# Kernel tuning notes

Measured on AMD Instinct MI355X. Metric: run time of the kernel, lower is better.

## Reference

```python
import jax, jax.numpy as jnp
import numpy as np

B, N, D_IN, D_OUT, MAX_POS = 256, 256, 768, 300, 256
NEG_INF = -9e15
LEAKY_SLOPE = 0.2


def setup_inputs() -> dict:
    key = jax.random.key(0)
    ks = jax.random.split(key, 6)
    h = jax.random.normal(ks[0], (B, N, D_IN), dtype=jnp.float32)
    adj = (jax.random.uniform(ks[1], (B, N, N)) > 0.9).astype(jnp.float32)
    adj = jnp.maximum(adj, jnp.eye(N, dtype=jnp.float32)[None])
    positions = jax.random.randint(ks[2], (B, N), 0, MAX_POS)
    W = jax.random.normal(ks[3], (D_IN, D_OUT), dtype=jnp.float32) * (1.0 / np.sqrt(D_IN))
    a_src = jax.random.normal(ks[4], (1, D_OUT), dtype=jnp.float32) * 0.05
    a_dst = jax.random.normal(ks[5], (1, D_OUT), dtype=jnp.float32) * 0.05
    pos_table = jax.random.normal(jax.random.fold_in(key, 7), (MAX_POS, D_OUT), dtype=jnp.float32)
    return {"h": h, "adj": adj, "positions": positions, "W": W,
            "a_src": a_src, "a_dst": a_dst, "pos_table": pos_table}


def reference(h, adj, positions, W, a_src, a_dst, pos_table):
    # Wh = W(h) + position embedding          [B, N, D_OUT]
    Wh = jnp.einsum('bni,io->bno', h, W) + pos_table[positions]
    # additive attention scores
    f_src = jnp.einsum('bno,o->bn', Wh, a_src[0])  # [B, N]
    f_dst = jnp.einsum('bno,o->bn', Wh, a_dst[0])  # [B, N]
    e = f_src[:, :, None] + f_dst[:, None, :]      # [B, N, N]
    e = jnp.where(e >= 0, e, LEAKY_SLOPE * e)      # LeakyReLU(0.2)
    # adjacency masking + softmax over last dim
    masked = jnp.where(adj > 0, e, NEG_INF)
    attention = jax.nn.softmax(masked, axis=-1)
    # (eval mode: edge dropout and dropout are identity)
    h_prime = jnp.einsum('bnm,bmo->bno', attention, Wh)
    return h_prime, attention
```

## Files before the change

kernel.cpp:

```cpp
#include <hip/hip_runtime.h>

#define B_    256
#define N_    256
#define DIN   768
#define DOUT  300
#define DOUTP 320
#define NT    20
#define M_    (B_*N_)
#define HP_ELEMS (M_*DOUT)
#define NEG_INF -9.0e15f

typedef _Float16 f16;
typedef __attribute__((ext_vector_type(8))) _Float16 f16x8;
typedef __attribute__((ext_vector_type(4))) _Float16 f16x4;
typedef __attribute__((ext_vector_type(4))) float    f32x4;

__device__ __forceinline__ void async_copy16(void* lds, const void* g) {
    __builtin_amdgcn_global_load_lds(
        (const __attribute__((address_space(1))) void*)g,
        (__attribute__((address_space(3))) void*)lds, 16, 0, 0);
}

__global__ __launch_bounds__(256) void prep_wt(const float* __restrict__ W,
                                               f16* __restrict__ Wt) {
    int idx = blockIdx.x * 256 + threadIdx.x;
    if (idx >= DOUTP * DIN) return;
    int n = idx / DIN, k = idx - n * DIN;
    float v = (n < DOUT) ? W[k * DOUT + n] : 0.0f;
    Wt[idx] = (f16)v;
}

__global__ __launch_bounds__(256, 3) void gemm1(
    const float* __restrict__ h, const f16* __restrict__ Wt,
    const int* __restrict__ positions,
    const float* __restrict__ a_src, const float* __restrict__ a_dst,
    const float* __restrict__ pos_table,
    f16* __restrict__ WhT, float* __restrict__ f_src, float* __restrict__ f_dst)
{
    __shared__ f16 Al[64 * 40];
    __shared__ f16 Bl[DOUTP * 32];
    __shared__ float pfs[64][2], pfd[64][2];

    const int tid  = threadIdx.x;
    const int wave = tid >> 6, lane = tid & 63;
    const int quad = lane >> 4, c = lane & 15;
    const int rh = wave & 1;
    const int chf = wave >> 1;
    const int rowbase = blockIdx.x * 64;

    const int brow = lane >> 2;
    const int bj   = (lane & 3) ^ (brow & 3);

    const int ar = tid >> 2, aj = tid & 3;

    f32x4 acc[2][10];
#pragma unroll
    for (int rt = 0; rt < 2; ++rt)
#pragma unroll
        for (int i = 0; i < 10; ++i) acc[rt][i] = (f32x4){0.f, 0.f, 0.f, 0.f};

    for (int kt = 0; kt < DIN / 32; ++kt) {
#pragma unroll
        for (int i = 0; i < 5; ++i) {
            int chk = wave + 4 * i;
            int n = chk * 16 + brow;
            async_copy16((char*)Bl + chk * 1024,
                         Wt + (size_t)n * DIN + kt * 32 + bj * 8);
        }
        {
            const float4* src = (const float4*)(h + (size_t)(rowbase + ar) * DIN + kt * 32 + aj * 8);
            float4 v0 = src[0], v1 = src[1];
            *(f16x8*)&Al[ar * 40 + aj * 8] =
                (f16x8){(f16)v0.x, (f16)v0.y, (f16)v0.z, (f16)v0.w,
                        (f16)v1.x, (f16)v1.y, (f16)v1.z, (f16)v1.w};
        }
        __syncthreads();

        f16x8 af0 = *(const f16x8*)&Al[(rh * 32 + c) * 40 + quad * 8];
        f16x8 af1 = *(const f16x8*)&Al[(rh * 32 + 16 + c) * 40 + quad * 8];
#pragma unroll
        for (int i = 0; i < 10; ++i) {
            int n = (chf * 10 + i) * 16 + c;
            f16x8 bf = *(const f16x8*)&Bl[n * 32 + (quad ^ (n & 3)) * 8];
            acc[0][i] = __builtin_amdgcn_mfma_f32_16x16x32_f16(af0, bf, acc[0][i], 0, 0, 0);
            acc[1][i] = __builtin_amdgcn_mfma_f32_16x16x32_f16(af1, bf, acc[1][i], 0, 0, 0);
        }
        __syncthreads();
    }

    const int bidx  = rowbase >> 8;
    const int mloc  = (rowbase & 255);

    int posr[2][4];
#pragma unroll
    for (int rt = 0; rt < 2; ++rt)
#pragma unroll
        for (int r = 0; r < 4; ++r)
            posr[rt][r] = positions[rowbase + rh * 32 + rt * 16 + quad * 4 + r];

    float fs[2][4] = {{0,0,0,0},{0,0,0,0}}, fd[2][4] = {{0,0,0,0},{0,0,0,0}};
#pragma unroll
    for (int i = 0; i < 10; ++i) {
        int col = (chf * 10 + i) * 16 + c;
        if (col < DOUT) {
            float as = a_src[col], ad = a_dst[col];
#pragma unroll
            for (int rt = 0; rt < 2; ++rt)
#pragma unroll
                for (int r = 0; r < 4; ++r) {
                    float v = acc[rt][i][r] + pos_table[posr[rt][r] * DOUT + col];
                    acc[rt][i][r] = v;
                    fs[rt][r] += v * as;
                    fd[rt][r] += v * ad;
                }
        } else {
#pragma unroll
            for (int rt = 0; rt < 2; ++rt)
#pragma unroll
                for (int r = 0; r < 4; ++r) acc[rt][i][r] = 0.0f;
        }
    }
#pragma unroll
    for (int off = 1; off < 16; off <<= 1) {
#pragma unroll
        for (int rt = 0; rt < 2; ++rt)
#pragma unroll
            for (int r = 0; r < 4; ++r) {
                fs[rt][r] += __shfl_xor(fs[rt][r], off, 16);
                fd[rt][r] += __shfl_xor(fd[rt][r], off, 16);
            }
    }
    if (c == 0) {
#pragma unroll
        for (int rt = 0; rt < 2; ++rt)
#pragma unroll
            for (int r = 0; r < 4; ++r) {
                int row = rh * 32 + rt * 16 + quad * 4 + r;
                pfs[row][chf] = fs[rt][r];
                pfd[row][chf] = fd[rt][r];
            }
    }
#pragma unroll
    for (int i = 0; i < 10; ++i) {
        int col = (chf * 10 + i) * 16 + c;
#pragma unroll
        for (int rt = 0; rt < 2; ++rt) {
            int mrow = mloc + rh * 32 + rt * 16 + quad * 4;
            f16x4 u = (f16x4){(f16)acc[rt][i][0], (f16)acc[rt][i][1],
                              (f16)acc[rt][i][2], (f16)acc[rt][i][3]};
            *(f16x4*)(WhT + ((size_t)bidx * DOUTP + col) * N_ + mrow) = u;
        }
    }
    __syncthreads();
    if (tid < 64) {
        f_src[rowbase + tid] = pfs[tid][0] + pfs[tid][1];
        f_dst[rowbase + tid] = pfd[tid][0] + pfd[tid][1];
    }
}

__global__ __launch_bounds__(256) void softmax_att(
    const float* __restrict__ adj, const float* __restrict__ f_src,
    const float* __restrict__ f_dst, float* __restrict__ att)
{
    const int wave = threadIdx.x >> 6, lane = threadIdx.x & 63;
    const int row = blockIdx.x * 4 + wave;
    const int b = row >> 8;

    float fs = f_src[row];
    float4 fd4 = *(const float4*)(f_dst + b * N_ + lane * 4);
    float4 a4  = *(const float4*)(adj + (size_t)row * N_ + lane * 4);

    float e[4];
    {
        float v;
        v = fs + fd4.x; v = v >= 0.f ? v : 0.2f * v; e[0] = a4.x > 0.f ? v : NEG_INF;
        v = fs + fd4.y; v = v >= 0.f ? v : 0.2f * v; e[1] = a4.y > 0.f ? v : NEG_INF;
        v = fs + fd4.z; v = v >= 0.f ? v : 0.2f * v; e[2] = a4.z > 0.f ? v : NEG_INF;
        v = fs + fd4.w; v = v >= 0.f ? v : 0.2f * v; e[3] = a4.w > 0.f ? v : NEG_INF;
    }
    float mx = fmaxf(fmaxf(e[0], e[1]), fmaxf(e[2], e[3]));
#pragma unroll
    for (int off = 1; off < 64; off <<= 1) mx = fmaxf(mx, __shfl_xor(mx, off, 64));

    float p[4], s = 0.f;
#pragma unroll
    for (int i = 0; i < 4; ++i) { p[i] = __expf(e[i] - mx); s += p[i]; }
#pragma unroll
    for (int off = 1; off < 64; off <<= 1) s += __shfl_xor(s, off, 64);

    float inv = 1.0f / s;
    *(float4*)(att + (size_t)row * N_ + lane * 4) =
        make_float4(p[0] * inv, p[1] * inv, p[2] * inv, p[3] * inv);
}

__global__ __launch_bounds__(256, 3) void gemm2(
    const float* __restrict__ att, const f16* __restrict__ WhT,
    float* __restrict__ hp)
{
    __shared__ f16 Al[64 * 40];
    __shared__ f16 Bl[DOUTP * 32];

    const int tid  = threadIdx.x;
    const int wave = tid >> 6, lane = tid & 63;
    const int quad = lane >> 4, c = lane & 15;
    const int rh = wave & 1;
    const int chf = wave >> 1;
    const int rowbase = blockIdx.x * 64;
    const int bidx = rowbase >> 8;

    const int brow = lane >> 2;
    const int bj   = (lane & 3) ^ (brow & 3);
    const int ar = tid >> 2, aj = tid & 3;

    f32x4 acc[2][10];
#pragma unroll
    for (int rt = 0; rt < 2; ++rt)
#pragma unroll
        for (int i = 0; i < 10; ++i) acc[rt][i] = (f32x4){0.f, 0.f, 0.f, 0.f};

    for (int kt = 0; kt < N_ / 32; ++kt) {
#pragma unroll
        for (int i = 0; i < 5; ++i) {
            int chk = wave + 4 * i;
            int n = chk * 16 + brow;
            async_copy16((char*)Bl + chk * 1024,
                         WhT + ((size_t)bidx * DOUTP + n) * N_ + kt * 32 + bj * 8);
        }
        {
            const float4* src = (const float4*)(att + (size_t)(rowbase + ar) * N_ + kt * 32 + aj * 8);
            float4 v0 = src[0], v1 = src[1];
            *(f16x8*)&Al[ar * 40 + aj * 8] =
                (f16x8){(f16)v0.x, (f16)v0.y, (f16)v0.z, (f16)v0.w,
                        (f16)v1.x, (f16)v1.y, (f16)v1.z, (f16)v1.w};
        }
        __syncthreads();

        f16x8 af0 = *(const f16x8*)&Al[(rh * 32 + c) * 40 + quad * 8];
        f16x8 af1 = *(const f16x8*)&Al[(rh * 32 + 16 + c) * 40 + quad * 8];
#pragma unroll
        for (int i = 0; i < 10; ++i) {
            int n = (chf * 10 + i) * 16 + c;
            f16x8 bf = *(const f16x8*)&Bl[n * 32 + (quad ^ (n & 3)) * 8];
            acc[0][i] = __builtin_amdgcn_mfma_f32_16x16x32_f16(af0, bf, acc[0][i], 0, 0, 0);
            acc[1][i] = __builtin_amdgcn_mfma_f32_16x16x32_f16(af1, bf, acc[1][i], 0, 0, 0);
        }
        __syncthreads();
    }

#pragma unroll
    for (int i = 0; i < 10; ++i) {
        int col = (chf * 10 + i) * 16 + c;
        if (col < DOUT) {
#pragma unroll
            for (int rt = 0; rt < 2; ++rt) {
                int row0 = rowbase + rh * 32 + rt * 16 + quad * 4;
#pragma unroll
                for (int r = 0; r < 4; ++r)
                    hp[(size_t)(row0 + r) * DOUT + col] = acc[rt][i][r];
            }
        }
    }
}

extern "C" void kernel_launch(void* const* d_in, const int* in_sizes, int n_in,
                              void* d_out, int out_size, void* d_ws, size_t ws_size,
                              hipStream_t stream)
{
    const float* h         = (const float*)d_in[0];
    const float* adj       = (const float*)d_in[1];
    const int*   positions = (const int*)d_in[2];
    const float* W         = (const float*)d_in[3];
    const float* a_src     = (const float*)d_in[4];
    const float* a_dst     = (const float*)d_in[5];
    const float* pos_table = (const float*)d_in[6];

    float* hp  = (float*)d_out;
    float* att = hp + HP_ELEMS;

    f16*   Wt    = (f16*)d_ws;
    f16*   WhT   = Wt + (size_t)DOUTP * DIN;
    float* f_src = (float*)(WhT + (size_t)B_ * DOUTP * N_);
    float* f_dst = f_src + M_;

    hipLaunchKernelGGL(prep_wt,     dim3((DOUTP * DIN + 255) / 256), dim3(256), 0, stream, W, Wt);
    hipLaunchKernelGGL(gemm1,       dim3(M_ / 64),  dim3(256), 0, stream,
                       h, Wt, positions, a_src, a_dst, pos_table, WhT, f_src, f_dst);
    hipLaunchKernelGGL(softmax_att, dim3(M_ / 4),   dim3(256), 0, stream, adj, f_src, f_dst, att);
    hipLaunchKernelGGL(gemm2,       dim3(M_ / 64),  dim3(256), 0, stream, att, WhT, hp);
}
```

Baseline: 471.8 us.

## Fuse softmax into second GEMM and double-buffer GEMM pipelines

The separate softmax kernel is merged into gemm2. Each block now computes the masked LeakyReLU softmax for its 64 rows, writes the attention to global memory, and keeps an f16 copy in LDS as the A operand, so att is no longer read back from global memory. Both GEMMs now double-buffer the weight/WhT tiles in LDS. gemm1 also loads h straight into registers with a three-stage prefetch instead of staging it through LDS. The price is more LDS and registers per block (gemm2 occupancy hint drops to 2) and less overlap within the softmax phase.

New measurement: 484.9 us. 2.8% more time.

```diff
diff --git a/kernel.cpp b/kernel.cpp
--- a/kernel.cpp
+++ b/kernel.cpp
@@ -5,7 +5,6 @@
 #define DIN   768
 #define DOUT  300
 #define DOUTP 320
-#define NT    20
 #define M_    (B_*N_)
 #define HP_ELEMS (M_*DOUT)
 #define NEG_INF -9.0e15f
@@ -19,6 +18,11 @@
     __builtin_amdgcn_global_load_lds(
         (const __attribute__((address_space(1))) void*)g,
         (__attribute__((address_space(3))) void*)lds, 16, 0, 0);
+}
+
+__device__ __forceinline__ f16x8 cvt8(float4 u, float4 v) {
+    return (f16x8){(f16)u.x,(f16)u.y,(f16)u.z,(f16)u.w,
+                   (f16)v.x,(f16)v.y,(f16)v.z,(f16)v.w};
 }
 
 __global__ __launch_bounds__(256) void prep_wt(const float* __restrict__ W,
@@ -37,21 +41,37 @@
     const float* __restrict__ pos_table,
     f16* __restrict__ WhT, float* __restrict__ f_src, float* __restrict__ f_dst)
 {
-    __shared__ f16 Al[64 * 40];
-    __shared__ f16 Bl[DOUTP * 32];
+    __shared__ f16 Bl[2][DOUTP * 32];
     __shared__ float pfs[64][2], pfd[64][2];
 
     const int tid  = threadIdx.x;
     const int wave = tid >> 6, lane = tid & 63;
     const int quad = lane >> 4, c = lane & 15;
-    const int rh = wave & 1;
-    const int chf = wave >> 1;
+    const int rh = wave & 1, chf = wave >> 1;
     const int rowbase = blockIdx.x * 64;
 
     const int brow = lane >> 2;
     const int bj   = (lane & 3) ^ (brow & 3);
 
-    const int ar = tid >> 2, aj = tid & 3;
+    const float* hrow0 = h + (size_t)(rowbase + rh * 32 + c) * DIN + quad * 8;
+    const float* hrow1 = hrow0 + 16 * DIN;
+
+    float4 a[3][4];
+
+#define LOAD_A(set, kt) do { \
+    const float4* p0 = (const float4*)(hrow0 + (kt) * 32); \
+    const float4* p1 = (const float4*)(hrow1 + (kt) * 32); \
+    a[set][0] = p0[0]; a[set][1] = p0[1]; \
+    a[set][2] = p1[0]; a[set][3] = p1[1]; } while (0)
+
+#define DMA_B(buf, kt) do { \
+    _Pragma("unroll") \
+    for (int i_ = 0; i_ < 5; ++i_) { \
+        int chk_ = wave + 4 * i_; \
+        int n_ = chk_ * 16 + brow; \
+        async_copy16((char*)Bl[buf] + chk_ * 1024, \
+                     Wt + (size_t)n_ * DIN + (kt) * 32 + bj * 8); \
+    } } while (0)
 
     f32x4 acc[2][10];
 #pragma unroll
@@ -59,37 +79,30 @@
 #pragma unroll
         for (int i = 0; i < 10; ++i) acc[rt][i] = (f32x4){0.f, 0.f, 0.f, 0.f};
 
-    for (int kt = 0; kt < DIN / 32; ++kt) {
-#pragma unroll
-        for (int i = 0; i < 5; ++i) {
-            int chk = wave + 4 * i;
-            int n = chk * 16 + brow;
-            async_copy16((char*)Bl + chk * 1024,
-                         Wt + (size_t)n * DIN + kt * 32 + bj * 8);
-        }
-        {
-            const float4* src = (const float4*)(h + (size_t)(rowbase + ar) * DIN + kt * 32 + aj * 8);
-            float4 v0 = src[0], v1 = src[1];
-            *(f16x8*)&Al[ar * 40 + aj * 8] =
-                (f16x8){(f16)v0.x, (f16)v0.y, (f16)v0.z, (f16)v0.w,
-                        (f16)v1.x, (f16)v1.y, (f16)v1.z, (f16)v1.w};
-        }
-        __syncthreads();
-
-        f16x8 af0 = *(const f16x8*)&Al[(rh * 32 + c) * 40 + quad * 8];
-        f16x8 af1 = *(const f16x8*)&Al[(rh * 32 + 16 + c) * 40 + quad * 8];
+    LOAD_A(0, 0); LOAD_A(1, 1);
+    DMA_B(0, 0);  DMA_B(1, 1);
+    __syncthreads();
+
+#pragma unroll
+    for (int kt = 0; kt < 24; ++kt) {
+        const int cur = kt & 1;
+        if (kt >= 1 && kt + 1 < 24) DMA_B(cur ^ 1, kt + 1);
+        if (kt + 2 < 24) LOAD_A((kt + 2) % 3, kt + 2);
+
+        f16x8 af0 = cvt8(a[kt % 3][0], a[kt % 3][1]);
+        f16x8 af1 = cvt8(a[kt % 3][2], a[kt % 3][3]);
 #pragma unroll
         for (int i = 0; i < 10; ++i) {
             int n = (chf * 10 + i) * 16 + c;
-            f16x8 bf = *(const f16x8*)&Bl[n * 32 + (quad ^ (n & 3)) * 8];
+            f16x8 bf = *(const f16x8*)&Bl[cur][n * 32 + (quad ^ (n & 3)) * 8];
             acc[0][i] = __builtin_amdgcn_mfma_f32_16x16x32_f16(af0, bf, acc[0][i], 0, 0, 0);
             acc[1][i] = __builtin_amdgcn_mfma_f32_16x16x32_f16(af1, bf, acc[1][i], 0, 0, 0);
         }
         __syncthreads();
     }
 
-    const int bidx  = rowbase >> 8;
-    const int mloc  = (rowbase & 255);
+    const int bidx = rowbase >> 8;
+    const int mloc = rowbase & 255;
 
     int posr[2][4];
 #pragma unroll
@@ -156,61 +169,91 @@
         f_src[rowbase + tid] = pfs[tid][0] + pfs[tid][1];
         f_dst[rowbase + tid] = pfd[tid][0] + pfd[tid][1];
     }
-}
-
-__global__ __launch_bounds__(256) void softmax_att(
+#undef LOAD_A
+#undef DMA_B
+}
+
+__global__ __launch_bounds__(256, 2) void gemm2(
     const float* __restrict__ adj, const float* __restrict__ f_src,
-    const float* __restrict__ f_dst, float* __restrict__ att)
+    const float* __restrict__ f_dst, const f16* __restrict__ WhT,
+    float* __restrict__ att, float* __restrict__ hp)
 {
-    const int wave = threadIdx.x >> 6, lane = threadIdx.x & 63;
-    const int row = blockIdx.x * 4 + wave;
-    const int b = row >> 8;
-
-    float fs = f_src[row];
-    float4 fd4 = *(const float4*)(f_dst + b * N_ + lane * 4);
-    float4 a4  = *(const float4*)(adj + (size_t)row * N_ + lane * 4);
-
-    float e[4];
-    {
-        float v;
-        v = fs + fd4.x; v = v >= 0.f ? v : 0.2f * v; e[0] = a4.x > 0.f ? v : NEG_INF;
-        v = fs + fd4.y; v = v >= 0.f ? v : 0.2f * v; e[1] = a4.y > 0.f ? v : NEG_INF;
-        v = fs + fd4.z; v = v >= 0.f ? v : 0.2f * v; e[2] = a4.z > 0.f ? v : NEG_INF;
-        v = fs + fd4.w; v = v >= 0.f ? v : 0.2f * v; e[3] = a4.w > 0.f ? v : NEG_INF;
-    }
-    float mx = fmaxf(fmaxf(e[0], e[1]), fmaxf(e[2], e[3]));
-#pragma unroll
-    for (int off = 1; off < 64; off <<= 1) mx = fmaxf(mx, __shfl_xor(mx, off, 64));
-
-    float p[4], s = 0.f;
-#pragma unroll
-    for (int i = 0; i < 4; ++i) { p[i] = __expf(e[i] - mx); s += p[i]; }
-#pragma unroll
-    for (int off = 1; off < 64; off <<= 1) s += __shfl_xor(s, off, 64);
-
-    float inv = 1.0f / s;
-    *(float4*)(att + (size_t)row * N_ + lane * 4) =
-        make_float4(p[0] * inv, p[1] * inv, p[2] * inv, p[3] * inv);
-}
-
-__global__ __launch_bounds__(256, 3) void gemm2(
-    const float* __restrict__ att, const f16* __restrict__ WhT,
-    float* __restrict__ hp)
-{
-    __shared__ f16 Al[64 * 40];
-    __shared__ f16 Bl[DOUTP * 32];
+    __shared__ f16 Al[64 * 264];
+    __shared__ f16 Bl[2][DOUTP * 32];
 
     const int tid  = threadIdx.x;
     const int wave = tid >> 6, lane = tid & 63;
     const int quad = lane >> 4, c = lane & 15;
-    const int rh = wave & 1;
-    const int chf = wave >> 1;
+    const int rh = wave & 1, chf = wave >> 1;
     const int rowbase = blockIdx.x * 64;
     const int bidx = rowbase >> 8;
 
     const int brow = lane >> 2;
     const int bj   = (lane & 3) ^ (brow & 3);
-    const int ar = tid >> 2, aj = tid & 3;
+
+#define DMA_B2(buf, kt) do { \
+    _Pragma("unroll") \
+    for (int i_ = 0; i_ < 5; ++i_) { \
+        int chk_ = wave + 4 * i_; \
+        int n_ = chk_ * 16 + brow; \
+        async_copy16((char*)Bl[buf] + chk_ * 1024, \
+                     WhT + ((size_t)bidx * DOUTP + n_) * N_ + (kt) * 32 + bj * 8); \
+    } } while (0)
+
+    DMA_B2(0, 0);
+    DMA_B2(1, 1);
+
+    const int sub = lane >> 4, l16 = lane & 15;
+
+    float4 fdv[4];
+#pragma unroll
+    for (int q = 0; q < 4; ++q)
+        fdv[q] = *(const float4*)(f_dst + bidx * N_ + q * 64 + l16 * 4);
+
+    float4 ar[4][4];
+    int rowg[4];
+#pragma unroll
+    for (int g = 0; g < 4; ++g) {
+        rowg[g] = rowbase + wave * 16 + g * 4 + sub;
+#pragma unroll
+        for (int q = 0; q < 4; ++q)
+            ar[g][q] = *(const float4*)(adj + (size_t)rowg[g] * N_ + q * 64 + l16 * 4);
+    }
+#pragma unroll
+    for (int g = 0; g < 4; ++g) {
+        float fs = f_src[rowg[g]];
+        float p[16];
+        float mx = -3.0e38f;
+#pragma unroll
+        for (int q = 0; q < 4; ++q) {
+            float vv[4] = {fs + fdv[q].x, fs + fdv[q].y, fs + fdv[q].z, fs + fdv[q].w};
+            float aa[4] = {ar[g][q].x, ar[g][q].y, ar[g][q].z, ar[g][q].w};
+#pragma unroll
+            for (int j = 0; j < 4; ++j) {
+                float v = vv[j];
+                v = v >= 0.f ? v : 0.2f * v;
+                v = aa[j] > 0.f ? v : NEG_INF;
+                p[q * 4 + j] = v;
+                mx = fmaxf(mx, v);
+            }
+        }
+#pragma unroll
+        for (int off = 1; off < 16; off <<= 1) mx = fmaxf(mx, __shfl_xor(mx, off, 16));
+        float s = 0.f;
+#pragma unroll
+        for (int j = 0; j < 16; ++j) { p[j] = __expf(p[j] - mx); s += p[j]; }
+#pragma unroll
+        for (int off = 1; off < 16; off <<= 1) s += __shfl_xor(s, off, 16);
+        float inv = 1.0f / s;
+        int lr = wave * 16 + g * 4 + sub;
+#pragma unroll
+        for (int q = 0; q < 4; ++q) {
+            float4 o = make_float4(p[q*4]*inv, p[q*4+1]*inv, p[q*4+2]*inv, p[q*4+3]*inv);
+            *(float4*)(att + (size_t)rowg[g] * N_ + q * 64 + l16 * 4) = o;
+            *(f16x4*)&Al[lr * 264 + q * 64 + l16 * 4] =
+                (f16x4){(f16)o.x, (f16)o.y, (f16)o.z, (f16)o.w};
+        }
+    }
 
     f32x4 acc[2][10];
 #pragma unroll
@@ -218,29 +261,19 @@
 #pragma unroll
         for (int i = 0; i < 10; ++i) acc[rt][i] = (f32x4){0.f, 0.f, 0.f, 0.f};
 
-    for (int kt = 0; kt < N_ / 32; ++kt) {
-#pragma unroll
-        for (int i = 0; i < 5; ++i) {
-            int chk = wave + 4 * i;
-            int n = chk * 16 + brow;
-            async_copy16((char*)Bl + chk * 1024,
-                         WhT + ((size_t)bidx * DOUTP + n) * N_ + kt * 32 + bj * 8);
-        }
-        {
-            const float4* src = (const float4*)(att + (size_t)(rowbase + ar) * N_ + kt * 32 + aj * 8);
-            float4 v0 = src[0], v1 = src[1];
-            *(f16x8*)&Al[ar * 40 + aj * 8] =
-                (f16x8){(f16)v0.x, (f16)v0.y, (f16)v0.z, (f16)v0.w,
-                        (f16)v1.x, (f16)v1.y, (f16)v1.z, (f16)v1.w};
-        }
-        __syncthreads();
-
-        f16x8 af0 = *(const f16x8*)&Al[(rh * 32 + c) * 40 + quad * 8];
-        f16x8 af1 = *(const f16x8*)&Al[(rh * 32 + 16 + c) * 40 + quad * 8];
+    __syncthreads();
+
+#pragma unroll
+    for (int kt = 0; kt < 8; ++kt) {
+        const int cur = kt & 1;
+        if (kt >= 1 && kt + 1 < 8) DMA_B2(cur ^ 1, kt + 1);
+
+        f16x8 af0 = *(const f16x8*)&Al[(rh * 32 + c) * 264 + kt * 32 + quad * 8];
+        f16x8 af1 = *(const f16x8*)&Al[(rh * 32 + 16 + c) * 264 + kt * 32 + quad * 8];
 #pragma unroll
         for (int i = 0; i < 10; ++i) {
             int n = (chf * 10 + i) * 16 + c;
-            f16x8 bf = *(const f16x8*)&Bl[n * 32 + (quad ^ (n & 3)) * 8];
+            f16x8 bf = *(const f16x8*)&Bl[cur][n * 32 + (quad ^ (n & 3)) * 8];
             acc[0][i] = __builtin_amdgcn_mfma_f32_16x16x32_f16(af0, bf, acc[0][i], 0, 0, 0);
             acc[1][i] = __builtin_amdgcn_mfma_f32_16x16x32_f16(af1, bf, acc[1][i], 0, 0, 0);
         }
@@ -260,6 +293,7 @@
             }
         }
     }
+#undef DMA_B2
 }
 
 extern "C" void kernel_launch(void* const* d_in, const int* in_sizes, int n_in,
@@ -282,9 +316,9 @@
     float* f_src = (float*)(WhT + (size_t)B_ * DOUTP * N_);
     float* f_dst = f_src + M_;
 
-    hipLaunchKernelGGL(prep_wt,     dim3((DOUTP * DIN + 255) / 256), dim3(256), 0, stream, W, Wt);
-    hipLaunchKernelGGL(gemm1,       dim3(M_ / 64),  dim3(256), 0, stream,
+    hipLaunchKernelGGL(prep_wt, dim3((DOUTP * DIN + 255) / 256), dim3(256), 0, stream, W, Wt);
+    hipLaunchKernelGGL(gemm1,   dim3(M_ / 64), dim3(256), 0, stream,
                        h, Wt, positions, a_src, a_dst, pos_table, WhT, f_src, f_dst);
-    hipLaunchKernelGGL(softmax_att, dim3(M_ / 4),   dim3(256), 0, stream, adj, f_src, f_dst, att);
-    hipLaunchKernelGGL(gemm2,       dim3(M_ / 64),  dim3(256), 0, stream, att, WhT, hp);
-}
+    hipLaunchKernelGGL(gemm2,   dim3(M_ / 64), dim3(256), 0, stream,
+                       adj, f_src, f_dst, WhT, att, hp);
+}
```
